# Performance work log

Hardware: AMD Instinct MI355X
Metric: run time of the kernel (lower is better)

## Reference

```python
import jax, jax.numpy as jnp
import numpy as np
from jax import lax

# Module config (matches init_kwargs): mode='swta', patchwise=True, w_nrm=True, k=1, alpha=1
COUT, CIN, KH, KW = 32, 16, 3, 3
STRIDE = 1
K_TEMP = 1.0


def setup_inputs() -> dict:
    key = jax.random.key(0)
    k1, k2 = jax.random.split(key)
    x = jax.random.normal(k1, (16, CIN, 256, 256), dtype=jnp.float32)
    # xavier_normal_: std = sqrt(2/(fan_in+fan_out)), fan_in=CIN*KH*KW, fan_out=COUT*KH*KW
    std = float(np.sqrt(2.0 / (CIN * KH * KW + COUT * KH * KW)))
    weight = jax.random.normal(k2, (COUT, CIN, KH, KW), dtype=jnp.float32) * std
    bias = jnp.zeros((COUT,), dtype=jnp.float32)
    return {"x": x, "weight": weight, "bias": bias}


def _unfold(x, kh, kw, sh, sw):
    # torch F.unfold: output [B, C*kh*kw, L], patch features ordered (c, kh, kw)
    B, C, H, W = x.shape
    Ho = (H - kh) // sh + 1
    Wo = (W - kw) // sw + 1
    cols = [x[:, :, i:i + (Ho - 1) * sh + 1:sh, j:j + (Wo - 1) * sw + 1:sw]
            for i in range(kh) for j in range(kw)]  # each [B,C,Ho,Wo]
    p = jnp.stack(cols, axis=2)  # [B, C, kh*kw, Ho, Wo]
    return p.reshape(B, C * kh * kw, Ho * Wo)


def reference(x, weight, bias):
    # --- compute_activation: weight-normalized conv2d (act = Identity) ---
    nrm = jnp.sqrt((weight ** 2).sum(axis=(1, 2, 3), keepdims=True))
    nrm = jnp.where(nrm == 0, jnp.ones_like(nrm), nrm)
    w = weight / nrm
    y = lax.conv_general_dilated(
        x, w, window_strides=(STRIDE, STRIDE), padding='VALID',
        dimension_numbers=('NCHW', 'OIHW', 'NCHW')) + bias[None, :, None, None]

    # --- SWTA Hebbian update (torch: under no_grad, stored into delta_w buffer) ---
    x_unf = _unfold(x, KH, KW, STRIDE, STRIDE)               # [B, CKK, L]
    x_flat = x_unf.transpose(0, 2, 1).reshape(-1, x_unf.shape[1])  # [B*L, CKK]
    r = jax.nn.softmax(y * K_TEMP, axis=1).transpose(1, 0, 2, 3)   # [O, B, Ho, Wo]
    r_sum = jnp.abs(r).sum(axis=(1, 2, 3), keepdims=True)
    r_sum = jnp.where(r_sum == 0, jnp.ones_like(r_sum), r_sum)
    cr = (jnp.abs(r) / r_sum) * r                             # [O, B, Ho, Wo]
    cr_flat = cr.reshape(COUT, -1)                            # [O, B*L]
    dec = cr_flat.sum(axis=1, keepdims=True) * weight.reshape(COUT, -1)
    delta_w = (cr_flat @ x_flat - dec).reshape(weight.shape)  # [O, CIN, KH, KW]

    return y, delta_w
```

## Files before the change

### kernel.cpp

```cpp
#include <hip/hip_runtime.h>


typedef unsigned short ushort_t;
typedef __attribute__((ext_vector_type(8)))  short  short8v;
typedef __attribute__((ext_vector_type(4)))  float  float4v;
typedef __attribute__((ext_vector_type(16))) float  float16v;

struct __attribute__((packed, aligned(4))) f4a { float x,y,z,w; };
struct __attribute__((packed, aligned(2))) u2a { ushort_t x,y; };

#define BATCH 16
#define CIN   16
#define H     256
#define W     256
#define HW    (H*W)
#define OCH   32
#define HO    254
#define WO    254
#define LPOS  (HO*WO)
#define YELEMS (BATCH*OCH*LPOS)
#define KFEAT 144
#define NROWS (BATCH*HO)
#define NCHUNK (NROWS*8)
#define GRIDA 1016
#define NSLAB GRIDA
#define NGRP  8
#define SLABS_PER_GRP 127

#define TCOLS 36

#define WS_RSUM 0
#define WS_R2   32
#define WS_ACC  64
#define WS_MODE 4672
#define WS_WNB  4680
#define WS_PART 8192
#define WS_PART2 (8192 + NSLAB*4608)
#define WS_NEED ((size_t)(WS_PART2 + NGRP*4608)*4)

__device__ __forceinline__ float bf2f(ushort_t u){
  union{unsigned u; float f;} c; c.u = ((unsigned)u) << 16; return c.f;
}
__device__ __forceinline__ ushort_t f2bf(float f){
  union{float f; unsigned u;} c; c.f = f;
  unsigned x = c.u;
  return (ushort_t)((x + 0x7fffu + ((x >> 16) & 1u)) >> 16);
}
__device__ __forceinline__ unsigned as_u(float f){
  union{float f; unsigned u;} c; c.f = f; return c.u;
}
__device__ __forceinline__ void gload_lds16(const float* g, void* l){
  __builtin_amdgcn_global_load_lds(
      (const __attribute__((address_space(1))) void*)g,
      (__attribute__((address_space(3))) void*)l, 16, 0, 0);
}

__global__ __launch_bounds__(256) void hebb_prep(const ushort_t* __restrict__ x,
                                                 const ushort_t* __restrict__ w,
                                                 int* __restrict__ mode,
                                                 float* __restrict__ ws){
  int tid = threadIdx.x;
  int bad = 0;
  for (int i = tid; i < 16384; i += 256){
    unsigned e = ((unsigned)x[i] >> 7) & 0xFFu;
    bad |= (e >= 0x8Cu) ? 1 : 0;
  }
  unsigned long long m = __ballot(bad);
  __shared__ unsigned long long sm[4];
  __shared__ int mode_s;
  int wv = tid >> 6;
  if ((tid & 63) == 0) sm[wv] = m;
  __syncthreads();
  if (tid == 0){
    int md = ((sm[0] | sm[1] | sm[2] | sm[3]) != 0ULL) ? 1 : 0;
    *mode = md; mode_s = md;
  }
  __syncthreads();
  const int fp32 = mode_s;
  const float* wf = (const float*)w;
  __shared__ float inv_s[OCH];
  if (tid < OCH){
    float s = 0.f;
    for (int k = 0; k < KFEAT; k++){
      float v = fp32 ? wf[tid*KFEAT + k] : bf2f(w[tid*KFEAT + k]);
      s += v*v;
    }
    float nrm = sqrtf(s);
    inv_s[tid] = (nrm == 0.f) ? 1.f : (1.f/nrm);
  }
  __syncthreads();
  ushort_t* wnb = (ushort_t*)(ws + WS_WNB);
  for (int i = tid; i < 4608; i += 256){
    int o = i & 31, rest = i >> 5;
    int ij = rest >> 4, c = rest & 15;
    int k = c*9 + ij;
    float v = fp32 ? wf[o*KFEAT + k] : bf2f(w[o*KFEAT + k]);
    wnb[i] = f2bf(v * inv_s[o]);
    ws[WS_ACC + i] = 0.f;
  }
  if (tid < 64) ws[WS_RSUM + tid] = 0.f;
}

__global__ __launch_bounds__(256, 2) void hebb_passAB(
    const void* __restrict__ xv_, const void* __restrict__ bias_,
    const int* __restrict__ mode, const float* __restrict__ ws,
    float* __restrict__ rsum_g, float* __restrict__ r2sum_g,
    void* __restrict__ yout_, float* __restrict__ partial, int do_hebb){
  const int fp32 = *mode;
  __shared__ __align__(16) float xtile[4][2][1792];
  __shared__ __align__(16) ushort_t r2t[4][32*40];
  __shared__ float red_s[64];
  float* redp = &xtile[0][0][0];
  int tid = threadIdx.x;
  if (tid < 64) red_s[tid] = 0.f;
  __syncthreads();
  int wave = tid >> 6, lane = tid & 63;
  int pos = lane & 31, half = lane >> 5;
  int quad = lane >> 4, l16 = lane & 15;

  const ushort_t* wnb = (const ushort_t*)(ws + WS_WNB);
  short8v wa[9];
  #pragma unroll
  for (int ij = 0; ij < 9; ij++){
    union{ushort_t s[8]; short8v v;} pk;
    #pragma unroll
    for (int i = 0; i < 8; i++)
      pk.s[i] = wnb[(ij*16 + half*8 + i)*32 + pos];
    wa[ij] = pk.v;
  }
  float bv[16];
  #pragma unroll
  for (int r = 0; r < 16; r++){
    int och = (r&3) + 8*(r>>2) + 4*half;
    bv[r] = fp32 ? ((const float*)bias_)[och] : bf2f(((const ushort_t*)bias_)[och]);
  }
  float rsA[16];
  #pragma unroll
  for (int r = 0; r < 16; r++) rsA[r] = 0.f;
  float r2B0 = 0.f, r2B1 = 0.f;

  int goff[7], qcol[7];
  #pragma unroll
  for (int i = 0; i < 7; i++){
    int slot = i*64 + lane; slot = (slot > 431) ? 431 : slot;
    int rr = slot/9, q = slot - 9*rr;
    int c = rr/3, ii = rr - 3*c;
    goff[i] = c*HW + ii*W;
    qcol[i] = q*4;
  }

  float4v hacc[18];
  #pragma unroll
  for (int i = 0; i < 18; i++) hacc[i] = (float4v){0.f,0.f,0.f,0.f};

  ushort_t* t2 = r2t[wave];
  const int cc0 = blockIdx.x*4 + wave;

  if (fp32){
    {
      int cc = __builtin_amdgcn_readfirstlane(cc0);
      int row = cc >> 3, sub = cc & 7;
      int b = row / HO, ho = row - b*HO, wo0 = sub << 5;
      const float* xb = (const float*)xv_ + (size_t)b*(CIN*HW) + (size_t)ho*W;
      char* twn = (char*)&xtile[wave][0][0];
      #pragma unroll
      for (int i = 0; i < 7; i++){
        int col = wo0 + qcol[i]; col = (col > 252) ? 252 : col;
        gload_lds16(xb + goff[i] + col, twn + i*1024);
      }
    }
    for (int kk = 0; kk < 8; kk++){
      int cc = __builtin_amdgcn_readfirstlane(cc0 + kk*(GRIDA*4));
      int row = cc >> 3, sub = cc & 7;
      int b = row / HO, ho = row - b*HO;
      int wo0 = sub << 5;
      int wo = wo0 + pos;
      float* tw = &xtile[wave][kk & 1][0];

      if (kk < 7){
        int cn = __builtin_amdgcn_readfirstlane(cc0 + (kk+1)*(GRIDA*4));
        int rown = cn >> 3, subn = cn & 7;
        int bn = rown / HO, hon = rown - bn*HO, won0 = subn << 5;
        const float* xbn = (const float*)xv_ + (size_t)bn*(CIN*HW) + (size_t)hon*W;
        char* twn = (char*)&xtile[wave][(kk+1) & 1][0];
        #pragma unroll
        for (int i = 0; i < 7; i++){
          int col = won0 + qcol[i]; col = (col > 252) ? 252 : col;
          gload_lds16(xbn + goff[i] + col, twn + i*1024);
        }
      }
      asm volatile("s_waitcnt vmcnt(7)" ::: "memory");

      float16v av;
      #pragma unroll
      for (int r = 0; r < 16; r++) av[r] = bv[r];

      #pragma unroll
      for (int ij = 0; ij < 9; ij++){
        const int ii = ij/3, jj = ij - 3*ii;
        unsigned g[8];
        #pragma unroll
        for (int i2 = 0; i2 < 8; i2++)
          g[i2] = as_u(tw[((half*8 + i2)*3 + ii)*TCOLS + pos + jj]) + 0x8000u;
        union{unsigned u[4]; short8v v;} pk;
        pk.u[0] = __builtin_amdgcn_perm(g[1], g[0], 0x07060302u);
        pk.u[1] = __builtin_amdgcn_perm(g[3], g[2], 0x07060302u);
        pk.u[2] = __builtin_amdgcn_perm(g[5], g[4], 0x07060302u);
        pk.u[3] = __builtin_amdgcn_perm(g[7], g[6], 0x07060302u);
        av = __builtin_amdgcn_mfma_f32_32x32x16_bf16(wa[ij], pk.v, av, 0, 0, 0);
      }

      int valid = (wo < WO) ? 1 : 0;
      if (valid){
        size_t yb = (size_t)b*(OCH*(size_t)LPOS) + (size_t)(half*4)*LPOS
                  + (size_t)ho*WO + wo;
        #pragma unroll
        for (int r = 0; r < 16; r++){
          size_t yi = yb + (size_t)(((r&3) + 8*(r>>2)))*LPOS;
          ((float*)yout_)[yi] = av[r];
        }
      }

      float m = -3.0e38f;
      #pragma unroll
      for (int r = 0; r < 16; r++) m = fmaxf(m, av[r]);
      m = fmaxf(m, __shfl_xor(m, 32));
      float s = 0.f;
      #pragma unroll
      for (int r = 0; r < 16; r++){ float e = __expf(av[r] - m); av[r] = e; s += e; }
      s += __shfl_xor(s, 32);
      float inv = valid ? (1.f/s) : 0.f;

      #pragma unroll
      for (int r = 0; r < 16; r++){
        float rr = av[r]*inv;
        rsA[r] += rr;
        int och = (r&3) + 8*(r>>2) + 4*half;
        t2[och*40 + pos] = f2bf(rr*rr);
      }

      short8v a0 = *(const short8v*)(t2 + l16*40      + quad*8);
      short8v a1 = *(const short8v*)(t2 + (16+l16)*40 + quad*8);
      {
        float p0 = 0.f, p1 = 0.f;
        #pragma unroll
        for (int i = 0; i < 8; i++){
          p0 += bf2f((ushort_t)a0[i]);
          p1 += bf2f((ushort_t)a1[i]);
        }
        r2B0 += p0; r2B1 += p1;
      }

      if (do_hebb){
        #pragma unroll
        for (int n = 0; n < 9; n++){
          int kh = n*16 + l16, c = kh/9, ij2 = kh - 9*c, ii = ij2/3, jj = ij2 - 3*ii;
          const float* hp = tw + (c*3 + ii)*TCOLS + jj + quad*8;
          unsigned f[8];
          #pragma unroll
          for (int i = 0; i < 8; i++) f[i] = as_u(hp[i]);
          union{unsigned u[4]; short8v v;} pk;
          pk.u[0] = __builtin_amdgcn_perm(f[1], f[0], 0x07060302u);
          pk.u[1] = __builtin_amdgcn_perm(f[3], f[2], 0x07060302u);
          pk.u[2] = __builtin_amdgcn_perm(f[5], f[4], 0x07060302u);
          pk.u[3] = __builtin_amdgcn_perm(f[7], f[6], 0x07060302u);
          hacc[n]   = __builtin_amdgcn_mfma_f32_16x16x32_bf16(a0, pk.v, hacc[n],   0,0,0);
          hacc[9+n] = __builtin_amdgcn_mfma_f32_16x16x32_bf16(a1, pk.v, hacc[9+n], 0,0,0);
        }
      }
    }
  } else {
    for (int kk = 0; kk < 8; kk++){
      int cc = __builtin_amdgcn_readfirstlane(cc0 + kk*(GRIDA*4));
      int row = cc >> 3, sub = cc & 7;
      int b = row / HO, ho = row - b*HO;
      int wo0 = sub << 5;
      int wo = wo0 + pos;
      int tail = (sub == 7);

      float16v av;
      #pragma unroll
      for (int r = 0; r < 16; r++) av[r] = bv[r];

      #pragma unroll
      for (int ij = 0; ij < 9; ij++){
        const int ii = ij/3, jj = ij - 3*ii;
        int wcol = wo + jj; wcol = (wcol < 256) ? wcol : 255;
        size_t a0i = (size_t)b*(CIN*HW) + (size_t)(half*8)*HW + (size_t)(ho+ii)*W + wcol;
        const ushort_t* xp = (const ushort_t*)xv_;
        union{ushort_t s[8]; short8v v;} pk;
        #pragma unroll
        for (int i2 = 0; i2 < 8; i2++)
          pk.s[i2] = xp[a0i + (size_t)i2*HW];
        av = __builtin_amdgcn_mfma_f32_32x32x16_bf16(wa[ij], pk.v, av, 0, 0, 0);
      }

      int valid = (wo < WO) ? 1 : 0;
      if (valid){
        size_t yb = (size_t)b*(OCH*(size_t)LPOS) + (size_t)(half*4)*LPOS
                  + (size_t)ho*WO + wo;
        #pragma unroll
        for (int r = 0; r < 16; r++){
          size_t yi = yb + (size_t)(((r&3) + 8*(r>>2)))*LPOS;
          ((ushort_t*)yout_)[yi] = f2bf(av[r]);
        }
      }

      float m = -3.0e38f;
      #pragma unroll
      for (int r = 0; r < 16; r++) m = fmaxf(m, av[r]);
      m = fmaxf(m, __shfl_xor(m, 32));
      float s = 0.f;
      #pragma unroll
      for (int r = 0; r < 16; r++){ float e = __expf(av[r] - m); av[r] = e; s += e; }
      s += __shfl_xor(s, 32);
      float inv = valid ? (1.f/s) : 0.f;

      #pragma unroll
      for (int r = 0; r < 16; r++){
        float rr = av[r]*inv;
        rsA[r] += rr;
        int och = (r&3) + 8*(r>>2) + 4*half;
        t2[och*40 + pos] = f2bf(rr*rr);
      }

      short8v a0 = *(const short8v*)(t2 + l16*40      + quad*8);
      short8v a1 = *(const short8v*)(t2 + (16+l16)*40 + quad*8);
      {
        float p0 = 0.f, p1 = 0.f;
        #pragma unroll
        for (int i = 0; i < 8; i++){
          p0 += bf2f((ushort_t)a0[i]);
          p1 += bf2f((ushort_t)a1[i]);
        }
        r2B0 += p0; r2B1 += p1;
      }

      if (do_hebb){
        int xbase = b*(CIN*HW) + ho*W + wo0;
        #pragma unroll
        for (int n = 0; n < 9; n++){
          int kh = n*16 + l16, c = kh/9, ij2 = kh - 9*c, ii = ij2/3, jj = ij2 - 3*ii;
          int ko = (c*H + ii)*W + jj;
          const ushort_t* xp = (const ushort_t*)xv_ + (size_t)(xbase + ko + quad*8);
          union{ushort_t s[8]; short8v v;} pk;
          if (tail && quad == 3){
            u2a u0 = *(const u2a*)xp, u1 = *(const u2a*)(xp+2), u2 = *(const u2a*)(xp+4);
            pk.s[0]=u0.x; pk.s[1]=u0.y; pk.s[2]=u1.x; pk.s[3]=u1.y;
            pk.s[4]=u2.x; pk.s[5]=u2.y; pk.s[6]=0; pk.s[7]=0;
          } else {
            u2a u0 = *(const u2a*)xp,   u1 = *(const u2a*)(xp+2);
            u2a u2 = *(const u2a*)(xp+4), u3 = *(const u2a*)(xp+6);
            pk.s[0]=u0.x; pk.s[1]=u0.y; pk.s[2]=u1.x; pk.s[3]=u1.y;
            pk.s[4]=u2.x; pk.s[5]=u2.y; pk.s[6]=u3.x; pk.s[7]=u3.y;
          }
          hacc[n]   = __builtin_amdgcn_mfma_f32_16x16x32_bf16(a0, pk.v, hacc[n],   0,0,0);
          hacc[9+n] = __builtin_amdgcn_mfma_f32_16x16x32_bf16(a1, pk.v, hacc[9+n], 0,0,0);
        }
      }
    }
  }

  #pragma unroll
  for (int r = 0; r < 16; r++){
    float a = rsA[r];
    #pragma unroll
    for (int off = 1; off < 32; off <<= 1)
      a += __shfl_xor(a, off);
    if (pos == 0){
      int och = (r&3) + 8*(r>>2) + 4*half;
      atomicAdd(&red_s[och], a);
    }
  }
  r2B0 += __shfl_xor(r2B0, 16); r2B0 += __shfl_xor(r2B0, 32);
  r2B1 += __shfl_xor(r2B1, 16); r2B1 += __shfl_xor(r2B1, 32);
  if (lane < 16){
    atomicAdd(&red_s[32 + lane],      r2B0);
    atomicAdd(&red_s[32 + 16 + lane], r2B1);
  }
  __syncthreads();
  if (tid < 32)      atomicAdd(rsum_g  + tid,      red_s[tid]);
  else if (tid < 64) atomicAdd(r2sum_g + (tid-32), red_s[tid]);

  if (do_hebb){
    for (int wv = 0; wv < 4; wv++){
      if (wave == wv){
        #pragma unroll
        for (int mi = 0; mi < 2; mi++)
          #pragma unroll
          for (int n = 0; n < 9; n++)
            #pragma unroll
            for (int rg = 0; rg < 4; rg++){
              int o  = mi*16 + quad*4 + rg;
              int kh = n*16 + l16;
              if (wv == 0) redp[o*KFEAT + kh]  = hacc[mi*9+n][rg];
              else         redp[o*KFEAT + kh] += hacc[mi*9+n][rg];
            }
      }
      __syncthreads();
    }
    float* myp = partial + (size_t)blockIdx.x*4608;
    for (int i = tid; i < 4608; i += 256) myp[i] = redp[i];
  }
}

__global__ __launch_bounds__(256) void hebb_red(const float* __restrict__ partial,
                                                float* __restrict__ partial2){
  int t = blockIdx.x*256 + threadIdx.x;
  if (t >= NGRP*4608) return;
  int g = t / 4608, col = t - g*4608;
  const float* p = partial + (size_t)g*SLABS_PER_GRP*4608 + col;
  float s0=0.f, s1=0.f, s2=0.f, s3=0.f;
  int j = 0;
  for (; j + 4 <= SLABS_PER_GRP; j += 4){
    s0 += p[(size_t)(j  )*4608];
    s1 += p[(size_t)(j+1)*4608];
    s2 += p[(size_t)(j+2)*4608];
    s3 += p[(size_t)(j+3)*4608];
  }
  for (; j < SLABS_PER_GRP; j++) s0 += p[(size_t)j*4608];
  partial2[t] = ((s0+s1)+(s2+s3));
}

template<int FP32>
__global__ __launch_bounds__(256) void hebb_passB_fb(
    const void* __restrict__ xv_, const int* __restrict__ mode,
    const float* __restrict__ ws, const void* __restrict__ ybf_,
    float* __restrict__ acc_g){
  if (*mode != FP32) return;
  __shared__ __align__(16) ushort_t crs[32*128];
  __shared__ __align__(16) ushort_t xs[144*128];
  __shared__ float rsinv_s[32];
  int tid = threadIdx.x;
  if (tid < 32){
    float rs = ws[WS_RSUM + tid];
    rsinv_s[tid] = (rs == 0.f) ? 1.f : (1.f/rs);
  }
  __syncthreads();

  float4v av[18];
  #pragma unroll
  for (int i = 0; i < 18; i++) av[i] = (float4v){0.f,0.f,0.f,0.f};
  int wave = tid >> 6, lane = tid & 63;
  int quad = lane >> 4, l16 = lane & 15;
  int t = tid & 127, kh0 = tid >> 7;

  for (int s = blockIdx.x; s < NROWS*2; s += (int)gridDim.x){
    int row = s >> 1, half = s & 1;
    int b = row / HO, ho = row - b*HO;
    int wo0 = half << 7;
    int tlen = half ? (WO - 128) : 128;
    size_t xoff = (size_t)b*(CIN*HW) + (size_t)ho*W + wo0;
    bool tvalid = t < tlen;

    #pragma unroll
    for (int it = 0; it < 72; it++){
      const int kh = 2*it + kh0;
      const int c = kh/9, ij = kh - 9*c, ii = ij/3, jj = ij - 3*ii;
      size_t gi = xoff + (size_t)(c*H + ii)*W + jj + t;
      ushort_t val;
      if (FP32) val = tvalid ? f2bf(((const float*)xv_)[gi]) : (ushort_t)0;
      else      val = tvalid ? ((const ushort_t*)xv_)[gi]    : (ushort_t)0;
      xs[kh*128 + t] = val;
    }
    if (tid < 128){
      if (tvalid){
        float r[32];
        size_t yb = (size_t)b*(OCH*(size_t)LPOS) + (size_t)ho*WO + wo0 + tid;
        float m = -3.0e38f;
        #pragma unroll
        for (int o = 0; o < 32; o++){
          float v = FP32 ? ((const float*)ybf_)[yb + (size_t)o*LPOS]
                         : bf2f(((const ushort_t*)ybf_)[yb + (size_t)o*LPOS]);
          r[o] = v; m = fmaxf(m, v);
        }
        float ssum = 0.f;
        #pragma unroll
        for (int o = 0; o < 32; o++){ r[o] = __expf(r[o]-m); ssum += r[o]; }
        float inv = 1.f/ssum;
        #pragma unroll
        for (int o = 0; o < 32; o++) r[o] *= inv;
        #pragma unroll
        for (int o = 0; o < 32; o++) crs[o*128 + tid] = f2bf(r[o]*r[o]*rsinv_s[o]);
      } else {
        #pragma unroll
        for (int o = 0; o < 32; o++) crs[o*128 + tid] = 0;
      }
    }
    __syncthreads();

    int t0 = wave*32;
    short8v a0 = *(const short8v*)(crs + l16*128      + t0 + quad*8);
    short8v a1 = *(const short8v*)(crs + (16+l16)*128 + t0 + quad*8);
    #pragma unroll
    for (int n = 0; n < 9; n++){
      short8v bfr = *(const short8v*)(xs + (n*16 + l16)*128 + t0 + quad*8);
      av[n]   = __builtin_amdgcn_mfma_f32_16x16x32_bf16(a0, bfr, av[n],   0,0,0);
      av[9+n] = __builtin_amdgcn_mfma_f32_16x16x32_bf16(a1, bfr, av[9+n], 0,0,0);
    }
    __syncthreads();
  }

  #pragma unroll
  for (int mi = 0; mi < 2; mi++)
    #pragma unroll
    for (int n = 0; n < 9; n++)
      #pragma unroll
      for (int rg = 0; rg < 4; rg++){
        int o  = mi*16 + quad*4 + rg;
        int kh = n*16 + l16;
        atomicAdd(acc_g + o*KFEAT + kh, av[mi*9+n][rg]);
      }
}

__global__ __launch_bounds__(256) void hebb_fin(const ushort_t* __restrict__ w,
    const int* __restrict__ mode, const float* __restrict__ ws,
    const float* __restrict__ partial2, int use_rbuf, void* __restrict__ dout){
  int tid = blockIdx.x*256 + threadIdx.x;
  if (tid >= 4608) return;
  const int fp32 = *mode;
  int o = tid / KFEAT;
  float rs = ws[WS_RSUM + o];
  rs = (rs == 0.f) ? 1.f : rs;
  float base;
  if (use_rbuf){
    float s = 0.f;
    #pragma unroll
    for (int j = 0; j < NGRP; j++)
      s += partial2[(size_t)j*4608 + tid];
    base = s / rs;
  } else {
    base = ws[WS_ACC + tid];
  }
  float crsum = ws[WS_R2 + o] / rs;
  float wv = fp32 ? ((const float*)w)[tid] : bf2f(w[tid]);
  float d = base - crsum * wv;
  if (fp32) ((float*)dout)[(size_t)YELEMS + tid] = d;
  else      ((ushort_t*)dout)[(size_t)YELEMS + tid] = f2bf(d);
}

extern "C" void kernel_launch(void* const* d_in, const int* in_sizes, int n_in,
                              void* d_out, int out_size, void* d_ws, size_t ws_size,
                              hipStream_t stream){
  const void* x    = d_in[0];
  const ushort_t* w = (const ushort_t*)d_in[1];
  const void* bias = d_in[2];
  float* ws   = (float*)d_ws;
  int*   mode = (int*)(ws + WS_MODE);
  float* part = ws + WS_PART;
  float* part2 = ws + WS_PART2;
  int use_rbuf = (ws_size >= WS_NEED) ? 1 : 0;

  hebb_prep<<<1, 256, 0, stream>>>((const ushort_t*)x, w, mode, ws);
  hebb_passAB<<<GRIDA, 256, 0, stream>>>(x, bias, mode, ws,
                                         ws + WS_RSUM, ws + WS_R2, d_out,
                                         part, use_rbuf);
  if (use_rbuf){
    hebb_red<<<144, 256, 0, stream>>>(part, part2);
  } else {
    hebb_passB_fb<0><<<512, 256, 0, stream>>>(x, mode, ws, d_out, ws + WS_ACC);
    hebb_passB_fb<1><<<512, 256, 0, stream>>>(x, mode, ws, d_out, ws + WS_ACC);
  }
  hebb_fin<<<18, 256, 0, stream>>>(w, mode, ws, part2, use_rbuf, d_out);
}
```

Baseline: 300.8 us.

## Template passAB on dtype, swizzle block order, unroll double-buffered prefetch loop

Turns the main kernel into a template on the input precision, so the fp32/bf16 branch is resolved at compile time. Both instantiations are launched and the one that does not match the mode exits early. Block IDs are swizzled so that consecutive blocks take spread-out chunk indices. The fp32 loop is manually unrolled by two with explicit A/B LDS buffers and deeper vmcnt waits, keeping more loads in flight. The cost is an extra kernel launch that exits immediately, plus more register and code size.

```diff
diff --git a/kernel.cpp b/kernel.cpp
--- a/kernel.cpp
+++ b/kernel.cpp
@@ -23,6 +23,7 @@
 #define NROWS (BATCH*HO)
 #define NCHUNK (NROWS*8)
 #define GRIDA 1016
+#define CSTEP (GRIDA*4)
 #define NSLAB GRIDA
 #define NGRP  8
 #define SLABS_PER_GRP 127
@@ -101,12 +102,13 @@
   if (tid < 64) ws[WS_RSUM + tid] = 0.f;
 }
 
+template<int FP32>
 __global__ __launch_bounds__(256, 2) void hebb_passAB(
     const void* __restrict__ xv_, const void* __restrict__ bias_,
     const int* __restrict__ mode, const float* __restrict__ ws,
     float* __restrict__ rsum_g, float* __restrict__ r2sum_g,
     void* __restrict__ yout_, float* __restrict__ partial, int do_hebb){
-  const int fp32 = *mode;
+  if (*mode != FP32) return;
   __shared__ __align__(16) float xtile[4][2][1792];
   __shared__ __align__(16) ushort_t r2t[4][32*40];
   __shared__ float red_s[64];
@@ -118,6 +120,9 @@
   int pos = lane & 31, half = lane >> 5;
   int quad = lane >> 4, l16 = lane & 15;
 
+  int bid = (int)blockIdx.x;
+  int swz = (bid & 7)*127 + (bid >> 3);
+
   const ushort_t* wnb = (const ushort_t*)(ws + WS_WNB);
   short8v wa[9];
   #pragma unroll
@@ -132,7 +137,7 @@
   #pragma unroll
   for (int r = 0; r < 16; r++){
     int och = (r&3) + 8*(r>>2) + 4*half;
-    bv[r] = fp32 ? ((const float*)bias_)[och] : bf2f(((const ushort_t*)bias_)[och]);
+    bv[r] = FP32 ? ((const float*)bias_)[och] : bf2f(((const ushort_t*)bias_)[och]);
   }
   float rsA[16];
   #pragma unroll
@@ -154,42 +159,30 @@
   for (int i = 0; i < 18; i++) hacc[i] = (float4v){0.f,0.f,0.f,0.f};
 
   ushort_t* t2 = r2t[wave];
-  const int cc0 = blockIdx.x*4 + wave;
-
-  if (fp32){
-    {
-      int cc = __builtin_amdgcn_readfirstlane(cc0);
-      int row = cc >> 3, sub = cc & 7;
+  const int cc0 = swz*4 + wave;
+
+  if (FP32){
+    float* twA = &xtile[wave][0][0];
+    float* twB = &xtile[wave][1][0];
+
+    auto stage = [&](int cc, float* dst){
+      int c2 = __builtin_amdgcn_readfirstlane(cc);
+      int row = c2 >> 3, sub = c2 & 7;
       int b = row / HO, ho = row - b*HO, wo0 = sub << 5;
       const float* xb = (const float*)xv_ + (size_t)b*(CIN*HW) + (size_t)ho*W;
-      char* twn = (char*)&xtile[wave][0][0];
       #pragma unroll
       for (int i = 0; i < 7; i++){
         int col = wo0 + qcol[i]; col = (col > 252) ? 252 : col;
-        gload_lds16(xb + goff[i] + col, twn + i*1024);
-      }
-    }
-    for (int kk = 0; kk < 8; kk++){
-      int cc = __builtin_amdgcn_readfirstlane(cc0 + kk*(GRIDA*4));
-      int row = cc >> 3, sub = cc & 7;
+        gload_lds16(xb + goff[i] + col, (char*)dst + i*1024);
+      }
+    };
+
+    auto body = [&](int cc, const float* tw){
+      int c2 = __builtin_amdgcn_readfirstlane(cc);
+      int row = c2 >> 3, sub = c2 & 7;
       int b = row / HO, ho = row - b*HO;
       int wo0 = sub << 5;
       int wo = wo0 + pos;
-      float* tw = &xtile[wave][kk & 1][0];
-
-      if (kk < 7){
-        int cn = __builtin_amdgcn_readfirstlane(cc0 + (kk+1)*(GRIDA*4));
-        int rown = cn >> 3, subn = cn & 7;
-        int bn = rown / HO, hon = rown - bn*HO, won0 = subn << 5;
-        const float* xbn = (const float*)xv_ + (size_t)bn*(CIN*HW) + (size_t)hon*W;
-        char* twn = (char*)&xtile[wave][(kk+1) & 1][0];
-        #pragma unroll
-        for (int i = 0; i < 7; i++){
-          int col = won0 + qcol[i]; col = (col > 252) ? 252 : col;
-          gload_lds16(xbn + goff[i] + col, twn + i*1024);
-        }
-      }
-      asm volatile("s_waitcnt vmcnt(7)" ::: "memory");
 
       float16v av;
       #pragma unroll
@@ -268,10 +261,27 @@
           hacc[9+n] = __builtin_amdgcn_mfma_f32_16x16x32_bf16(a1, pk.v, hacc[9+n], 0,0,0);
         }
       }
+    };
+
+    stage(cc0, twA);
+    for (int j = 0; j < 4; j++){
+      int cA = cc0 + (2*j)*CSTEP;
+      int cB = cA + CSTEP;
+      stage(cB, twB);
+      if (j == 0) asm volatile("s_waitcnt vmcnt(7)"  ::: "memory");
+      else        asm volatile("s_waitcnt vmcnt(23)" ::: "memory");
+      body(cA, twA);
+      if (j < 3){
+        stage(cB + CSTEP, twA);
+        asm volatile("s_waitcnt vmcnt(23)" ::: "memory");
+      } else {
+        asm volatile("s_waitcnt vmcnt(16)" ::: "memory");
+      }
+      body(cB, twB);
     }
   } else {
     for (int kk = 0; kk < 8; kk++){
-      int cc = __builtin_amdgcn_readfirstlane(cc0 + kk*(GRIDA*4));
+      int cc = __builtin_amdgcn_readfirstlane(cc0 + kk*CSTEP);
       int row = cc >> 3, sub = cc & 7;
       int b = row / HO, ho = row - b*HO;
       int wo0 = sub << 5;
@@ -552,9 +562,12 @@
   int use_rbuf = (ws_size >= WS_NEED) ? 1 : 0;
 
   hebb_prep<<<1, 256, 0, stream>>>((const ushort_t*)x, w, mode, ws);
-  hebb_passAB<<<GRIDA, 256, 0, stream>>>(x, bias, mode, ws,
-                                         ws + WS_RSUM, ws + WS_R2, d_out,
-                                         part, use_rbuf);
+  hebb_passAB<0><<<GRIDA, 256, 0, stream>>>(x, bias, mode, ws,
+                                            ws + WS_RSUM, ws + WS_R2, d_out,
+                                            part, use_rbuf);
+  hebb_passAB<1><<<GRIDA, 256, 0, stream>>>(x, bias, mode, ws,
+                                            ws + WS_RSUM, ws + WS_R2, d_out,
+                                            part, use_rbuf);
   if (use_rbuf){
     hebb_red<<<144, 256, 0, stream>>>(part, part2);
   } else {
```

Measured after the change: 299.9 us. Within noise of the previous version (-0.3%).
